# Kernel tuning notes

Hardware: AMD Instinct MI355X
Metric: run time of the kernel (lower is better)

## Reference

```python
import jax, jax.numpy as jnp
import numpy as np
import math

B, S, D, H = 8, 512, 1024, 16
HD = D // H  # 64
FF = 4 * D
EPS = 1e-5


def setup_inputs() -> dict:
    key = jax.random.key(0)
    ks = jax.random.split(key, 12)
    sc = 0.02
    return {
        "x":   jax.random.normal(ks[0], (B, S, D), jnp.float32),
        "Wq":  jax.random.normal(ks[1], (H, D, HD), jnp.float32) * sc,
        "Wk":  jax.random.normal(ks[2], (H, D, HD), jnp.float32) * sc,
        "Wv":  jax.random.normal(ks[3], (H, D, HD), jnp.float32) * sc,
        "Wo":  jax.random.normal(ks[4], (D, D), jnp.float32) * sc,
        "bo":  jnp.zeros((D,), jnp.float32),
        "g1":  jnp.ones((D,), jnp.float32),
        "b1":  jnp.zeros((D,), jnp.float32),
        "g2":  jnp.ones((D,), jnp.float32),
        "b2":  jnp.zeros((D,), jnp.float32),
        "W1":  jax.random.normal(ks[5], (D, FF), jnp.float32) * sc,
        "bf1": jnp.zeros((FF,), jnp.float32),
        "W2":  jax.random.normal(ks[6], (FF, D), jnp.float32) * sc,
        "bf2": jnp.zeros((D,), jnp.float32),
    }


def _layernorm(x, gamma, beta):
    # biased variance, matches torch.var(correction=0)
    mean = jnp.mean(x, axis=-1, keepdims=True)
    var = jnp.mean((x - mean) ** 2, axis=-1, keepdims=True)
    return (x - mean) / jnp.sqrt(var + EPS) * gamma + beta


def _block(x, Wq, Wk, Wv, Wo, bo, g1, b1, g2, b2, W1, bf1, W2, bf2):
    h = _layernorm(x, g1, b1)
    # per-head projections (no bias): [B,H,S,HD]
    Q = jnp.einsum("bsd,hde->bhse", h, Wq)
    K = jnp.einsum("bsd,hde->bhse", h, Wk)
    V = jnp.einsum("bsd,hde->bhse", h, Wv)
    scores = jnp.einsum("bhse,bhte->bhst", Q, K) / math.sqrt(HD)
    causal = jnp.triu(jnp.ones((S, S), bool), k=1)  # upper-triangular masked
    scores = jnp.where(causal, jnp.float32(-1e10), scores)
    att = jax.nn.softmax(scores, axis=-1)  # dropout in eval mode = identity
    ctx = jnp.einsum("bhst,bhte->bhse", att, V)
    # concat heads in order -> [B,S,D]
    ctx = ctx.transpose(0, 2, 1, 3).reshape(B, S, D)
    attn_out = ctx @ Wo + bo
    cache = attn_out + x
    h2 = _layernorm(cache, g2, b2)
    ff = jax.nn.gelu(h2 @ W1 + bf1, approximate=False) @ W2 + bf2
    return ff + cache


def reference(x, Wq, Wk, Wv, Wo, bo, g1, b1, g2, b2, W1, bf1, W2, bf2):
    return _block(x, Wq, Wk, Wv, Wo, bo, g1, b1, g2, b2, W1, bf1, W2, bf2)
```

## Files before the change

### kernel.cpp

```cpp
#include <hip/hip_runtime.h>
#include <hip/hip_bf16.h>

typedef __hip_bfloat16 bf16;

#define B_   8
#define S_   512
#define D_   1024
#define H_   16
#define HD_  64
#define FF_  4096
#define ROWS (B_ * S_)

typedef __attribute__((ext_vector_type(8))) unsigned short u16x8;
typedef __attribute__((ext_vector_type(4))) float f32x4;

typedef __attribute__((address_space(1))) const unsigned int GU32;
typedef __attribute__((address_space(3))) unsigned int LU32;
__device__ __forceinline__ void gld16(const void* g, void* l) {
    __builtin_amdgcn_global_load_lds((GU32*)g, (LU32*)l, 16, 0, 0);
}

__device__ __forceinline__ float bf2f(unsigned short u) {
    union { unsigned int i; float f; } v; v.i = ((unsigned int)u) << 16; return v.f;
}
__device__ __forceinline__ unsigned short f2bfu(float f) {
    bf16 h = __float2bfloat16(f);
    return *reinterpret_cast<unsigned short*>(&h);
}
__device__ __forceinline__ float ldsel(const void* p, size_t i, bool f32) {
    return f32 ? ((const float*)p)[i]
               : __bfloat162float(((const bf16*)p)[i]);
}
__device__ __forceinline__ float gelu_exact(float x) {
    return 0.5f * x * (1.f + erff(x * 0.70710678118654752440f));
}

__global__ __launch_bounds__(256) void ln_kernel(const void* __restrict__ x,
                                                 const void* __restrict__ gam,
                                                 const void* __restrict__ bet,
                                                 bf16* __restrict__ out,
                                                 int x_ws,
                                                 const unsigned short* __restrict__ probe) {
    bool pf32 = (probe[0] == 0);
    bool xf32 = (!x_ws) && pf32;
    int row = blockIdx.x;
    int tid = threadIdx.x;
    size_t rb = (size_t)row * D_;
    float v[4];
#pragma unroll
    for (int i = 0; i < 4; ++i) v[i] = ldsel(x, rb + tid + i * 256, xf32);
    float s  = v[0] + v[1] + v[2] + v[3];
    float s2 = v[0] * v[0] + v[1] * v[1] + v[2] * v[2] + v[3] * v[3];
#pragma unroll
    for (int off = 32; off > 0; off >>= 1) {
        s  += __shfl_down(s, off);
        s2 += __shfl_down(s2, off);
    }
    __shared__ float red[8];
    int wv = tid >> 6, ln = tid & 63;
    if (ln == 0) { red[wv] = s; red[4 + wv] = s2; }
    __syncthreads();
    s  = red[0] + red[1] + red[2] + red[3];
    s2 = red[4] + red[5] + red[6] + red[7];
    float mean = s * (1.f / 1024.f);
    float var  = s2 * (1.f / 1024.f) - mean * mean;
    float rstd = rsqrtf(var + 1e-5f);
#pragma unroll
    for (int i = 0; i < 4; ++i) {
        int c = tid + i * 256;
        float g = ldsel(gam, c, pf32), b = ldsel(bet, c, pf32);
        out[rb + c] = __float2bfloat16((v[i] - mean) * rstd * g + b);
    }
}

__global__ __launch_bounds__(256) void transpose_kernel(
    const void* __restrict__ src, bf16* __restrict__ dst,
    int N, int K, int sK, int sH,
    const unsigned short* __restrict__ probe) {
    bool pf32 = (probe[0] == 0);
    int tilesN = N >> 6;
    int tn = blockIdx.x % tilesN, tk = blockIdx.x / tilesN;
    int n0 = tn * 64, k0 = tk * 64;
    __shared__ float T[64][65];
    int t = threadIdx.x;
    size_t headoff = (size_t)(n0 >> 6) * sH;
#pragma unroll
    for (int i = 0; i < 16; ++i) {
        int lin = t + i * 256;
        int kl = lin >> 6, nl = lin & 63;
        size_t e = headoff + (size_t)(k0 + kl) * sK + nl;
        T[kl][nl] = ldsel(src, e, pf32);
    }
    __syncthreads();
#pragma unroll
    for (int i = 0; i < 16; ++i) {
        int lin = t + i * 256;
        int nl = lin >> 6, kl = lin & 63;
        dst[(size_t)(n0 + nl) * K + k0 + kl] = __float2bfloat16(T[kl][nl]);
    }
}

template<int BN>
__global__ __launch_bounds__(256) void gemm_mfma(
    const bf16* __restrict__ A, const bf16* __restrict__ Bt,
    int K, int nSeg, int segShift, size_t segStride,
    const void* __restrict__ bias,
    const void* __restrict__ resid, int resid_ws,
    bf16* __restrict__ outWS, void* __restrict__ outFinal, int mode,
    const unsigned short* __restrict__ probe) {
    constexpr int BM  = 128;
    constexpr int NR  = BN / 32;
    constexpr int CH  = 8 + BN / 16;
    constexpr int NCH = CH / 4;
    bool pf32 = (probe[0] == 0);
    __shared__ alignas(16) unsigned short As[BM * 32];
    __shared__ alignas(16) unsigned short Bs[BN * 32];
    int tid  = threadIdx.x;
    int lane = tid & 63, wv = tid >> 6;
    int g = lane >> 4, i16 = lane & 15;
    int wrow = wv >> 1, wcol = wv & 1;
    int m0 = blockIdx.y * BM, n0 = blockIdx.x * BN;

    f32x4 acc[4][NR];
#pragma unroll
    for (int i = 0; i < 4; ++i)
#pragma unroll
        for (int j = 0; j < NR; ++j) acc[i][j] = (f32x4){0.f, 0.f, 0.f, 0.f};

    const unsigned short* gsrc[NCH];
    unsigned short* ldst[NCH];
    {
        int rl = lane >> 2, kq = (lane & 3) * 8;
#pragma unroll
        for (int c0 = 0; c0 < NCH; ++c0) {
            int c = c0 * 4 + wv;
            if (c < 8) {
                gsrc[c0] = (const unsigned short*)A + (size_t)(m0 + c * 16 + rl) * K + kq;
                ldst[c0] = &As[c * 512];
            } else {
                gsrc[c0] = (const unsigned short*)Bt + (size_t)(n0 + (c - 8) * 16 + rl) * K + kq;
                ldst[c0] = &Bs[(c - 8) * 512];
            }
        }
    }

    for (int k0 = 0; k0 < K; k0 += 32) {
        __syncthreads();
#pragma unroll
        for (int c0 = 0; c0 < NCH; ++c0)
            gld16(gsrc[c0] + k0, ldst[c0]);
        __syncthreads();
        u16x8 af[4], bf[NR];
#pragma unroll
        for (int i = 0; i < 4; ++i)
            af[i] = *reinterpret_cast<const u16x8*>(&As[(wrow * 64 + i * 16 + i16) * 32 + g * 8]);
#pragma unroll
        for (int j = 0; j < NR; ++j)
            bf[j] = *reinterpret_cast<const u16x8*>(&Bs[(wcol * (BN / 2) + j * 16 + i16) * 32 + g * 8]);
#pragma unroll
        for (int i = 0; i < 4; ++i)
#pragma unroll
            for (int j = 0; j < NR; ++j)
                asm("v_mfma_f32_16x16x32_bf16 %0, %1, %2, %0"
                    : "+v"(acc[i][j]) : "v"(af[i]), "v"(bf[j]));
    }
    __builtin_amdgcn_sched_barrier(0);
    asm volatile("s_nop 7\n\ts_nop 7\n\ts_nop 7" ::: );
    __builtin_amdgcn_sched_barrier(0);

    int coll = i16, rowl = g * 4;
#pragma unroll
    for (int j = 0; j < NR; ++j) {
        int n = n0 + wcol * (BN / 2) + j * 16 + coll;
        int seg = n >> segShift;
        int nl = n & (nSeg - 1);
        float bval = (mode != 0) ? ldsel(bias, nl, pf32) : 0.f;
        bf16* ows = outWS + (size_t)seg * segStride;
#pragma unroll
        for (int i = 0; i < 4; ++i) {
            int mb = m0 + wrow * 64 + i * 16 + rowl;
#pragma unroll
            for (int r = 0; r < 4; ++r) {
                size_t idx = (size_t)(mb + r) * nSeg + nl;
                float c = acc[i][j][r];
                if (mode == 1) {
                    c += bval;
                    c += resid_ws ? __bfloat162float(((const bf16*)resid)[idx])
                                  : ldsel(resid, idx, pf32);
                } else if (mode == 2) {
                    c = gelu_exact(c + bval);
                }
                if (outFinal) {
                    if (pf32) ((float*)outFinal)[idx] = c;
                    else      ((bf16*)outFinal)[idx] = __float2bfloat16(c);
                } else {
                    ows[idx] = __float2bfloat16(c);
                }
            }
        }
    }
}

__global__ __launch_bounds__(256) void attn_kernel(const bf16* __restrict__ Qg,
                                                   const bf16* __restrict__ Kg,
                                                   const bf16* __restrict__ Vg,
                                                   bf16* __restrict__ Og) {
    constexpr int P = 72;
    __shared__ alignas(16) unsigned short Ks[64 * P];
    __shared__ alignas(16) unsigned short Vt[64 * P];
    __shared__ alignas(16) unsigned short Ps[64 * P];
    int qb = blockIdx.x;
    int bh = blockIdx.y;
    int b = bh >> 4, h = bh & 15;
    int tid = threadIdx.x;
    int lane = tid & 63, wv = tid >> 6;
    int g = lane >> 4, i16 = lane & 15;
    size_t base = ((size_t)b * S_) * D_ + h * HD_;

    u16x8 qa[2];
    {
        const unsigned short* qp = (const unsigned short*)Qg + base
            + (size_t)(qb * 64 + wv * 16 + i16) * D_ + g * 8;
#pragma unroll
        for (int kk = 0; kk < 2; ++kk) {
            u16x8 v = *reinterpret_cast<const u16x8*>(qp + kk * 32);
#pragma unroll
            for (int e = 0; e < 8; ++e) v[e] = f2bfu(bf2f(v[e]) * 0.125f);
            qa[kk] = v;
        }
    }
    f32x4 ov[4];
#pragma unroll
    for (int dj = 0; dj < 4; ++dj) ov[dj] = (f32x4){0.f, 0.f, 0.f, 0.f};
    float mrow[4], lrow[4];
#pragma unroll
    for (int r = 0; r < 4; ++r) { mrow[r] = -1e30f; lrow[r] = 0.f; }

    int st = tid >> 2, sd = (tid & 3) * 16;
    const unsigned short* Kp = (const unsigned short*)Kg + base + (size_t)st * D_ + sd;
    const unsigned short* Vp = (const unsigned short*)Vg + base + (size_t)st * D_ + sd;
    unsigned short* KsW = &Ks[st * P + sd];
    unsigned short* VtW = &Vt[sd * P + (st ^ sd)];
    int g1 = g >> 1, g0 = g & 1;
    unsigned short* PsW = &Ps[(wv * 16 + g * 4) * P + (i16 ^ (g0 << 3))];
    const unsigned short* PsR = &Ps[(wv * 16 + i16) * P + ((g ^ ((i16 >> 2) & 3)) << 3)];

    for (int kb = 0; kb <= qb; ++kb) {
        __syncthreads();
        size_t ko = (size_t)kb * 64 * D_;
        u16x8 k0 = *reinterpret_cast<const u16x8*>(Kp + ko);
        u16x8 k1 = *reinterpret_cast<const u16x8*>(Kp + ko + 8);
        u16x8 v0 = *reinterpret_cast<const u16x8*>(Vp + ko);
        u16x8 v1 = *reinterpret_cast<const u16x8*>(Vp + ko + 8);
        *reinterpret_cast<u16x8*>(KsW)     = k0;
        *reinterpret_cast<u16x8*>(KsW + 8) = k1;
#pragma unroll
        for (int ii = 0; ii < 8; ++ii) VtW[ii * P] = v0[ii];
#pragma unroll
        for (int ii = 0; ii < 8; ++ii) VtW[(ii + 8) * P] = v1[ii];
        __syncthreads();

        f32x4 sc[4];
#pragma unroll
        for (int tj = 0; tj < 4; ++tj) sc[tj] = (f32x4){0.f, 0.f, 0.f, 0.f};
#pragma unroll
        for (int kk = 0; kk < 2; ++kk)
#pragma unroll
            for (int tj = 0; tj < 4; ++tj) {
                u16x8 kf = *reinterpret_cast<const u16x8*>(
                    &Ks[(tj * 16 + i16) * P + kk * 32 + g * 8]);
                asm("v_mfma_f32_16x16x32_bf16 %0, %1, %2, %0"
                    : "+v"(sc[tj]) : "v"(qa[kk]), "v"(kf));
            }
        __builtin_amdgcn_sched_barrier(0);
        asm volatile("s_nop 7\n\ts_nop 7\n\ts_nop 7" ::: );
        __builtin_amdgcn_sched_barrier(0);

        if (kb == qb) {
#pragma unroll
            for (int tj = 0; tj < 4; ++tj)
#pragma unroll
                for (int r = 0; r < 4; ++r)
                    if (tj * 16 + i16 > wv * 16 + g * 4 + r) sc[tj][r] = -1e30f;
        }
        float al[4];
#pragma unroll
        for (int r = 0; r < 4; ++r) {
            float mt = fmaxf(fmaxf(sc[0][r], sc[1][r]), fmaxf(sc[2][r], sc[3][r]));
            mt = fmaxf(mt, __shfl_xor(mt, 1));
            mt = fmaxf(mt, __shfl_xor(mt, 2));
            mt = fmaxf(mt, __shfl_xor(mt, 4));
            mt = fmaxf(mt, __shfl_xor(mt, 8));
            float mnew = fmaxf(mrow[r], mt);
            al[r] = __expf(mrow[r] - mnew);
            mrow[r] = mnew;
        }
        float psum[4] = {0.f, 0.f, 0.f, 0.f};
        unsigned short pw[4][4];
#pragma unroll
        for (int tj = 0; tj < 4; ++tj)
#pragma unroll
            for (int r = 0; r < 4; ++r) {
                float p = __expf(sc[tj][r] - mrow[r]);
                unsigned short pb = f2bfu(p);
                pw[tj][r] = pb;
                psum[r] += bf2f(pb);
            }
#pragma unroll
        for (int r = 0; r < 4; ++r) {
            float ps = psum[r];
            ps += __shfl_xor(ps, 1);
            ps += __shfl_xor(ps, 2);
            ps += __shfl_xor(ps, 4);
            ps += __shfl_xor(ps, 8);
            lrow[r] = lrow[r] * al[r] + ps;
        }
#pragma unroll
        for (int dj = 0; dj < 4; ++dj)
#pragma unroll
            for (int r = 0; r < 4; ++r) ov[dj][r] *= al[r];
#pragma unroll
        for (int r = 0; r < 4; ++r)
#pragma unroll
            for (int tj = 0; tj < 4; ++tj)
                PsW[r * P + ((tj ^ g1) << 4)] = pw[tj][r];
#pragma unroll
        for (int kk = 0; kk < 2; ++kk) {
            u16x8 pf = *reinterpret_cast<const u16x8*>(PsR + kk * 32);
#pragma unroll
            for (int dj = 0; dj < 4; ++dj) {
                int tcol = ((kk << 5) | (g << 3)) ^ (dj << 4);
                u16x8 vf = *reinterpret_cast<const u16x8*>(
                    &Vt[(dj * 16 + i16) * P + tcol]);
                asm("v_mfma_f32_16x16x32_bf16 %0, %1, %2, %0"
                    : "+v"(ov[dj]) : "v"(pf), "v"(vf));
            }
        }
    }
    __builtin_amdgcn_sched_barrier(0);
    asm volatile("s_nop 7\n\ts_nop 7\n\ts_nop 7" ::: );
    __builtin_amdgcn_sched_barrier(0);
    float rl[4];
#pragma unroll
    for (int r = 0; r < 4; ++r) rl[r] = 1.f / lrow[r];
    bf16* op = Og + base + (size_t)(qb * 64 + wv * 16 + g * 4) * D_ + i16;
#pragma unroll
    for (int r = 0; r < 4; ++r)
#pragma unroll
        for (int dj = 0; dj < 4; ++dj)
            op[(size_t)r * D_ + dj * 16] = __float2bfloat16(ov[dj][r] * rl[r]);
}

extern "C" void kernel_launch(void* const* d_in, const int* in_sizes, int n_in,
                              void* d_out, int out_size, void* d_ws, size_t ws_size,
                              hipStream_t stream) {
    const void* x   = d_in[0];
    const void* Wq  = d_in[1];
    const void* Wk  = d_in[2];
    const void* Wv  = d_in[3];
    const void* Wo  = d_in[4];
    const void* bo  = d_in[5];
    const void* g1  = d_in[6];
    const void* b1  = d_in[7];
    const void* g2  = d_in[8];
    const void* b2  = d_in[9];
    const void* W1  = d_in[10];
    const void* bf1 = d_in[11];
    const void* W2  = d_in[12];
    const void* bf2 = d_in[13];
    const unsigned short* probe = (const unsigned short*)g1;

    bf16* ws = (bf16*)d_ws;
    const size_t Mi = (size_t)1024 * 1024;
    bf16* h     = ws;
    bf16* Qb    = ws + 4 * Mi;
    bf16* Kb    = ws + 8 * Mi;
    bf16* Vb    = ws + 12 * Mi;
    bf16* ctx   = ws;
    bf16* cache = ws + 4 * Mi;
    bf16* h2    = ws + 8 * Mi;
    bf16* ff1   = ws + 12 * Mi;
    bf16* WqT   = ws + 16 * Mi;
    bf16* WkT   = ws + 17 * Mi;
    bf16* WvT   = ws + 18 * Mi;
    bf16* WoT   = ws + 19 * Mi;
    bf16* W1T   = ws;
    bf16* W2T   = ws + 8 * Mi;

    transpose_kernel<<<256, 256, 0, stream>>>(Wq, WqT, 1024, 1024, HD_, D_ * HD_, probe);
    transpose_kernel<<<256, 256, 0, stream>>>(Wk, WkT, 1024, 1024, HD_, D_ * HD_, probe);
    transpose_kernel<<<256, 256, 0, stream>>>(Wv, WvT, 1024, 1024, HD_, D_ * HD_, probe);
    transpose_kernel<<<256, 256, 0, stream>>>(Wo, WoT, 1024, 1024, 1024, 64, probe);
    ln_kernel<<<ROWS, 256, 0, stream>>>(x, g1, b1, h, 0, probe);
    gemm_mfma<128><<<dim3(3072 / 128, ROWS / 128), 256, 0, stream>>>(
        h, WqT, 1024, 1024, 10, 4 * Mi,
        nullptr, nullptr, 0, Qb, nullptr, 0, probe);
    dim3 gA(S_ / 64, B_ * H_);
    attn_kernel<<<gA, 256, 0, stream>>>(Qb, Kb, Vb, ctx);
    gemm_mfma<64><<<dim3(1024 / 64, ROWS / 128), 256, 0, stream>>>(
        ctx, WoT, 1024, 1024, 30, 0,
        bo, x, 0, cache, nullptr, 1, probe);
    transpose_kernel<<<1024, 256, 0, stream>>>(W1, W1T, 4096, 1024, FF_, 64, probe);
    ln_kernel<<<ROWS, 256, 0, stream>>>(cache, g2, b2, h2, 1, probe);
    gemm_mfma<128><<<dim3(4096 / 128, ROWS / 128), 256, 0, stream>>>(
        h2, W1T, 1024, 4096, 30, 0,
        bf1, nullptr, 0, ff1, nullptr, 2, probe);
    transpose_kernel<<<1024, 256, 0, stream>>>(W2, W2T, 1024, 4096, 1024, 64, probe);
    gemm_mfma<64><<<dim3(1024 / 64, ROWS / 128), 256, 0, stream>>>(
        ff1, W2T, 4096, 1024, 30, 0,
        bf2, cache, 1, nullptr, d_out, 1, probe);
}
```

Measured before the change: 433.3 us.

## Double-buffer LDS tiles in MFMA GEMM and swizzle block order

```diff
diff --git a/kernel.cpp b/kernel.cpp
--- a/kernel.cpp
+++ b/kernel.cpp
@@ -113,13 +113,19 @@
     constexpr int CH  = 8 + BN / 16;
     constexpr int NCH = CH / 4;
     bool pf32 = (probe[0] == 0);
-    __shared__ alignas(16) unsigned short As[BM * 32];
-    __shared__ alignas(16) unsigned short Bs[BN * 32];
+    __shared__ alignas(16) unsigned short As[2][BM * 32];
+    __shared__ alignas(16) unsigned short Bs[2][BN * 32];
     int tid  = threadIdx.x;
     int lane = tid & 63, wv = tid >> 6;
     int g = lane >> 4, i16 = lane & 15;
     int wrow = wv >> 1, wcol = wv & 1;
-    int m0 = blockIdx.y * BM, n0 = blockIdx.x * BN;
+
+    int GX = gridDim.x;
+    int total = GX * gridDim.y;
+    int bid = blockIdx.y * GX + blockIdx.x;
+    int swz = bid;
+    if ((total & 7) == 0) swz = (bid & 7) * (total >> 3) + (bid >> 3);
+    int m0 = (swz / GX) * BM, n0 = (swz % GX) * BN;
 
     f32x4 acc[4][NR];
 #pragma unroll
@@ -128,7 +134,8 @@
         for (int j = 0; j < NR; ++j) acc[i][j] = (f32x4){0.f, 0.f, 0.f, 0.f};
 
     const unsigned short* gsrc[NCH];
-    unsigned short* ldst[NCH];
+    unsigned short* l0[NCH];
+    unsigned short* l1[NCH];
     {
         int rl = lane >> 2, kq = (lane & 3) * 8;
 #pragma unroll
@@ -136,34 +143,49 @@
             int c = c0 * 4 + wv;
             if (c < 8) {
                 gsrc[c0] = (const unsigned short*)A + (size_t)(m0 + c * 16 + rl) * K + kq;
-                ldst[c0] = &As[c * 512];
+                l0[c0] = &As[0][c * 512];
+                l1[c0] = &As[1][c * 512];
             } else {
                 gsrc[c0] = (const unsigned short*)Bt + (size_t)(n0 + (c - 8) * 16 + rl) * K + kq;
-                ldst[c0] = &Bs[(c - 8) * 512];
+                l0[c0] = &Bs[0][(c - 8) * 512];
+                l1[c0] = &Bs[1][(c - 8) * 512];
             }
         }
     }
 
-    for (int k0 = 0; k0 < K; k0 += 32) {
+#define STAGE0(KOFF) { _Pragma("unroll") \
+    for (int c0 = 0; c0 < NCH; ++c0) gld16(gsrc[c0] + (KOFF), l0[c0]); }
+#define STAGE1(KOFF) { _Pragma("unroll") \
+    for (int c0 = 0; c0 < NCH; ++c0) gld16(gsrc[c0] + (KOFF), l1[c0]); }
+#define COMPUTE(BUF) { \
+    u16x8 af[4], bfv[NR]; \
+    _Pragma("unroll") \
+    for (int i = 0; i < 4; ++i) \
+        af[i] = *reinterpret_cast<const u16x8*>(&As[BUF][(wrow * 64 + i * 16 + i16) * 32 + g * 8]); \
+    _Pragma("unroll") \
+    for (int j = 0; j < NR; ++j) \
+        bfv[j] = *reinterpret_cast<const u16x8*>(&Bs[BUF][(wcol * (BN / 2) + j * 16 + i16) * 32 + g * 8]); \
+    _Pragma("unroll") \
+    for (int i = 0; i < 4; ++i) \
+        _Pragma("unroll") \
+        for (int j = 0; j < NR; ++j) \
+            asm("v_mfma_f32_16x16x32_bf16 %0, %1, %2, %0" \
+                : "+v"(acc[i][j]) : "v"(af[i]), "v"(bfv[j])); }
+
+    STAGE0(0);
+    __syncthreads();
+    for (int k0 = 0; k0 < K; k0 += 64) {
+        STAGE1(k0 + 32);
+        COMPUTE(0);
         __syncthreads();
-#pragma unroll
-        for (int c0 = 0; c0 < NCH; ++c0)
-            gld16(gsrc[c0] + k0, ldst[c0]);
+        if (k0 + 64 < K) STAGE0(k0 + 64);
+        COMPUTE(1);
         __syncthreads();
-        u16x8 af[4], bf[NR];
-#pragma unroll
-        for (int i = 0; i < 4; ++i)
-            af[i] = *reinterpret_cast<const u16x8*>(&As[(wrow * 64 + i * 16 + i16) * 32 + g * 8]);
-#pragma unroll
-        for (int j = 0; j < NR; ++j)
-            bf[j] = *reinterpret_cast<const u16x8*>(&Bs[(wcol * (BN / 2) + j * 16 + i16) * 32 + g * 8]);
-#pragma unroll
-        for (int i = 0; i < 4; ++i)
-#pragma unroll
-            for (int j = 0; j < NR; ++j)
-                asm("v_mfma_f32_16x16x32_bf16 %0, %1, %2, %0"
-                    : "+v"(acc[i][j]) : "v"(af[i]), "v"(bf[j]));
-    }
+    }
+#undef STAGE0
+#undef STAGE1
+#undef COMPUTE
+
     __builtin_amdgcn_sched_barrier(0);
     asm volatile("s_nop 7\n\ts_nop 7\n\ts_nop 7" ::: );
     __builtin_amdgcn_sched_barrier(0);
```

Measured after the change: 430.4 us. About the same (-0.7%).
